# Kernel optimization log

Hardware: AMD Instinct MI355X
Metric: run time of the kernel (lower is better)

The kernel has to match this reference:

```python
import jax, jax.numpy as jnp
import numpy as np

IN_F = 2048
OUT_F = 2048
G = 5 + 3  # grid_size + spline_order
BATCH = 8192


def setup_inputs() -> dict:
    key = jax.random.key(0)
    k1, k2, k3 = jax.random.split(key, 3)
    x = jax.random.normal(k1, (BATCH, IN_F), dtype=jnp.float32)
    # kaiming_uniform(a=sqrt(5)) on (out,in): bound = 1/sqrt(in)
    bound = 1.0 / np.sqrt(IN_F)
    base_weight = jax.random.uniform(k2, (OUT_F, IN_F), dtype=jnp.float32,
                                     minval=-bound, maxval=bound)
    grid = 0.1 * jax.random.normal(k3, (IN_F, OUT_F, G), dtype=jnp.float32)
    return {"x": x, "base_weight": base_weight, "grid": grid}


def reference(x, base_weight, grid):
    # base branch: standard linear  (B, out)
    base_out = x @ base_weight.T
    # spline branch: Gaussian basis around the scalar grid mean  (B, in)
    basis = jnp.exp(-jnp.square(x - grid.mean()))
    # contract over in_features and the grid dim: sum_i sum_g basis[b,i]*grid[i,o,g]
    spline_out = basis @ grid.sum(axis=-1)  # (B, out)
    return base_out + spline_out
```

## Files before the change

kernel.cpp:

```cpp
#include <hip/hip_runtime.h>

#define IN_F   2048
#define OUT_F  2048
#define GDIM   8
#define BATCH  8192
#define KDIM   4096
#define GRID_TOTAL_INV (1.0f / 33554432.0f)

#define BK     32
#define NT     (KDIM / BK)
#define SLOT   32768
#define ATILE  16384

typedef __bf16 bf16x8 __attribute__((ext_vector_type(8)));
typedef float  f32x4  __attribute__((ext_vector_type(4)));
typedef unsigned short u16x8 __attribute__((ext_vector_type(8)));

__device__ __forceinline__ unsigned short f2bf(float f) {
  union { float f; unsigned int u; } v; v.f = f;
  unsigned int r = v.u + 0x7fffu + ((v.u >> 16) & 1u);
  return (unsigned short)(r >> 16);
}

__device__ __forceinline__ void gload_lds16(const void* g, void* l) {
  __builtin_amdgcn_global_load_lds(
      (const __attribute__((address_space(1))) void*)g,
      (__attribute__((address_space(3))) void*)l, 16, 0, 0);
}

template<int VM>
__device__ __forceinline__ void wait_vm() {
  if constexpr (VM == 12)     asm volatile("s_waitcnt vmcnt(12)" ::: "memory");
  else if constexpr (VM == 8) asm volatile("s_waitcnt vmcnt(8)"  ::: "memory");
  else if constexpr (VM == 4) asm volatile("s_waitcnt vmcnt(4)"  ::: "memory");
  else                        asm volatile("s_waitcnt vmcnt(0)"  ::: "memory");
}

__global__ __launch_bounds__(256) void prep_bw(const float* __restrict__ bw,
                                               unsigned short* __restrict__ Bt,
                                               float* __restrict__ sum_ptr) {
  if (blockIdx.x == 0 && threadIdx.x == 0) *sum_ptr = 0.0f;
  size_t i8 = ((size_t)blockIdx.x * 256 + threadIdx.x) * 8;
  const float4* p = reinterpret_cast<const float4*>(bw + i8);
  float4 a = p[0], b = p[1];
  u16x8 v;
  v[0] = f2bf(a.x); v[1] = f2bf(a.y); v[2] = f2bf(a.z); v[3] = f2bf(a.w);
  v[4] = f2bf(b.x); v[5] = f2bf(b.y); v[6] = f2bf(b.z); v[7] = f2bf(b.w);
  size_t o = i8 >> 11;
  size_t k = i8 & 2047;
  *reinterpret_cast<u16x8*>(Bt + o * KDIM + k) = v;
}

__global__ __launch_bounds__(256) void prep_grid(const float* __restrict__ grid,
                                                 unsigned short* __restrict__ Bt,
                                                 float* __restrict__ sum_ptr) {
  __shared__ float tile[32][33];
  __shared__ float wsum[4];
  int bi = blockIdx.x >> 6;
  int bo = blockIdx.x & 63;
  int i0 = bi << 5, o0 = bo << 5;
  int t = threadIdx.x;
  float local = 0.f;
#pragma unroll
  for (int p = 0; p < 4; ++p) {
    int li = t + 256 * p;
    int il = li >> 5, ol = li & 31;
    const float4* g4 = reinterpret_cast<const float4*>(
        grid + ((size_t)(i0 + il) * OUT_F + (size_t)(o0 + ol)) * GDIM);
    float4 a = g4[0], b = g4[1];
    float s = ((a.x + a.y) + (a.z + a.w)) + ((b.x + b.y) + (b.z + b.w));
    tile[il][ol] = s;
    local += s;
  }
#pragma unroll
  for (int off = 32; off >= 1; off >>= 1) local += __shfl_down(local, off, 64);
  int lane = t & 63, w = t >> 6;
  if (lane == 0) wsum[w] = local;
  __syncthreads();
#pragma unroll
  for (int p = 0; p < 4; ++p) {
    int li = t + 256 * p;
    int ol = li >> 5, il = li & 31;
    Bt[(size_t)(o0 + ol) * KDIM + IN_F + (i0 + il)] = f2bf(tile[il][ol]);
  }
  if (t == 0) atomicAdd(sum_ptr, (wsum[0] + wsum[1]) + (wsum[2] + wsum[3]));
}

__global__ __launch_bounds__(256) void prep_A(const float* __restrict__ x,
                                              const float* __restrict__ sum_ptr,
                                              unsigned short* __restrict__ Abuf) {
  float m = *sum_ptr * GRID_TOTAL_INV;
  size_t i8 = ((size_t)blockIdx.x * 256 + threadIdx.x) * 8;
  const float4* p = reinterpret_cast<const float4*>(x + i8);
  float4 a = p[0], b = p[1];
  float xs[8] = {a.x, a.y, a.z, a.w, b.x, b.y, b.z, b.w};
  u16x8 xv, bv;
#pragma unroll
  for (int j = 0; j < 8; ++j) {
    xv[j] = f2bf(xs[j]);
    float d = xs[j] - m;
    bv[j] = f2bf(__expf(-d * d));
  }
  size_t bi = i8 >> 11;
  size_t k  = i8 & 2047;
  *reinterpret_cast<u16x8*>(Abuf + bi * KDIM + k) = xv;
  *reinterpret_cast<u16x8*>(Abuf + bi * KDIM + IN_F + k) = bv;
}

__global__ __launch_bounds__(512, 2) void gemm_kernel(
    const unsigned short* __restrict__ A,
    const unsigned short* __restrict__ B,
    float* __restrict__ C) {
  __shared__ __align__(16) char lds[4 * SLOT];
  const int t    = threadIdx.x;
  const int lane = t & 63;
  const int wid  = t >> 6;
  const int wm   = wid >> 2;
  const int wn   = wid & 3;
  const int bx = blockIdx.x;
  const int bm = ((bx & 7) << 2) | ((bx >> 3) & 3);
  const int bn = bx >> 5;

  f32x4 acc[8][4] = {};

  const int cs = (t & 3) ^ ((t >> 4) & 3);
  const unsigned short* aSrc = A + ((size_t)(bm * 256 + (t >> 2)) * KDIM) + cs * 8;
  const unsigned short* bSrc = B + ((size_t)(bn * 256 + (t >> 2)) * KDIM) + cs * 8;
  const int dstOff = t * 16;

  const int swz = (lane >> 2) & 3;
  const int aRd = (wm * 128 + (lane & 15)) * 64 + (((lane >> 4) ^ swz) * 16);
  const int bRd = (wn * 64  + (lane & 15)) * 64 + (((lane >> 4) ^ swz) * 16);

  auto STAGE = [&](int tile) {
    const int slot = (tile & 3) * SLOT;
    const unsigned short* a = aSrc + tile * BK;
    const unsigned short* b = bSrc + tile * BK;
    gload_lds16(a,                        lds + slot + dstOff);
    gload_lds16(a + 128 * KDIM,           lds + slot + 8192 + dstOff);
    gload_lds16(b,                        lds + slot + ATILE + dstOff);
    gload_lds16(b + 128 * KDIM,           lds + slot + ATILE + 8192 + dstOff);
  };

  auto BODY = [&](int slotbase) {
    __builtin_amdgcn_sched_barrier(0);
    const char* sa = lds + slotbase + aRd;
    const char* sb = lds + slotbase + ATILE + bRd;
    bf16x8 af[8], bf[4];
#pragma unroll
    for (int m = 0; m < 8; ++m)
      af[m] = *reinterpret_cast<const bf16x8*>(sa + m * 1024);
#pragma unroll
    for (int n = 0; n < 4; ++n)
      bf[n] = *reinterpret_cast<const bf16x8*>(sb + n * 1024);
    asm volatile("s_waitcnt lgkmcnt(0)" ::: "memory");
    __builtin_amdgcn_sched_barrier(0);
    __builtin_amdgcn_s_barrier();
    __builtin_amdgcn_s_setprio(1);
#pragma unroll
    for (int m = 0; m < 8; ++m)
#pragma unroll
      for (int n = 0; n < 4; ++n)
        acc[m][n] = __builtin_amdgcn_mfma_f32_16x16x32_bf16(af[m], bf[n], acc[m][n], 0, 0, 0);
    __builtin_amdgcn_s_setprio(0);
  };

  STAGE(0); STAGE(1); STAGE(2);

  for (int kt = 0; kt < NT - 3; ++kt) {
    STAGE(kt + 3);
    wait_vm<12>();
    __builtin_amdgcn_s_barrier();
    BODY((kt & 3) * SLOT);
  }
  wait_vm<8>(); __builtin_amdgcn_s_barrier(); BODY(((NT - 3) & 3) * SLOT);
  wait_vm<4>(); __builtin_amdgcn_s_barrier(); BODY(((NT - 2) & 3) * SLOT);
  wait_vm<0>(); __builtin_amdgcn_s_barrier(); BODY(((NT - 1) & 3) * SLOT);

  const int rg = lane >> 4, cc = lane & 15;
  const size_t crow0 = (size_t)bm * 256 + wm * 128;
  const size_t ccol0 = (size_t)bn * 256 + wn * 64;
#pragma unroll
  for (int m = 0; m < 8; ++m)
#pragma unroll
    for (int n = 0; n < 4; ++n)
#pragma unroll
      for (int rr = 0; rr < 4; ++rr) {
        size_t row = crow0 + (size_t)m * 16 + rg * 4 + rr;
        size_t col = ccol0 + (size_t)n * 16 + cc;
        C[row * OUT_F + col] = acc[m][n][rr];
      }
}

extern "C" void kernel_launch(void* const* d_in, const int* in_sizes, int n_in,
                              void* d_out, int out_size, void* d_ws, size_t ws_size,
                              hipStream_t stream) {
  const float* x    = (const float*)d_in[0];
  const float* bw   = (const float*)d_in[1];
  const float* grid = (const float*)d_in[2];
  float* out = (float*)d_out;

  unsigned short* Abuf = (unsigned short*)d_ws;
  unsigned short* Bt   = Abuf + (size_t)BATCH * KDIM;
  float* sum_ptr = (float*)(Bt + (size_t)OUT_F * KDIM);

  prep_bw  <<<(OUT_F * IN_F / 8) / 256, 256, 0, stream>>>(bw, Bt, sum_ptr);
  prep_grid<<<64 * 64,                  256, 0, stream>>>(grid, Bt, sum_ptr);
  prep_A   <<<(BATCH * IN_F / 8) / 256, 256, 0, stream>>>(x, sum_ptr, Abuf);
  gemm_kernel<<<256, 512, 0, stream>>>(Abuf, Bt, out);
}
```

Measured before the change: 416.5 us.

## Restructure GEMM mainloop into double-buffered BK=64 pipeline with interleaved LDS reads

Replaces the 4-slot BK=32 ring buffer with two 64KB buffers holding BK=64 tiles, each split into two 32-wide subregions. Global-to-LDS loads for the next tile are interleaved with the ds_reads and MFMA quarters of the current tile, and A fragments are read in halves to cut register use. The intent is to halve the barriers per K element and overlap memory issue with compute more finely. The catch is a shallower prefetch depth (one tile ahead) and more complex vmcnt accounting, which could hurt correctness or latency hiding.

```diff
diff --git a/kernel.cpp b/kernel.cpp
--- a/kernel.cpp
+++ b/kernel.cpp
@@ -7,10 +7,11 @@
 #define KDIM   4096
 #define GRID_TOTAL_INV (1.0f / 33554432.0f)
 
-#define BK     32
-#define NT     (KDIM / BK)
-#define SLOT   32768
-#define ATILE  16384
+#define BK     64
+#define NKT    (KDIM / BK)
+#define BUFSZ  65536
+#define BOFF   32768
+#define REG    16384
 
 typedef __bf16 bf16x8 __attribute__((ext_vector_type(8)));
 typedef float  f32x4  __attribute__((ext_vector_type(4)));
@@ -26,14 +27,6 @@
   __builtin_amdgcn_global_load_lds(
       (const __attribute__((address_space(1))) void*)g,
       (__attribute__((address_space(3))) void*)l, 16, 0, 0);
-}
-
-template<int VM>
-__device__ __forceinline__ void wait_vm() {
-  if constexpr (VM == 12)     asm volatile("s_waitcnt vmcnt(12)" ::: "memory");
-  else if constexpr (VM == 8) asm volatile("s_waitcnt vmcnt(8)"  ::: "memory");
-  else if constexpr (VM == 4) asm volatile("s_waitcnt vmcnt(4)"  ::: "memory");
-  else                        asm volatile("s_waitcnt vmcnt(0)"  ::: "memory");
 }
 
 __global__ __launch_bounds__(256) void prep_bw(const float* __restrict__ bw,
@@ -111,7 +104,7 @@
     const unsigned short* __restrict__ A,
     const unsigned short* __restrict__ B,
     float* __restrict__ C) {
-  __shared__ __align__(16) char lds[4 * SLOT];
+  __shared__ __align__(16) char lds[2 * BUFSZ];
   const int t    = threadIdx.x;
   const int lane = t & 63;
   const int wid  = t >> 6;
@@ -122,60 +115,87 @@
   const int bn = bx >> 5;
 
   f32x4 acc[8][4] = {};
+  bf16x8 af[4], bf[4];
 
   const int cs = (t & 3) ^ ((t >> 4) & 3);
-  const unsigned short* aSrc = A + ((size_t)(bm * 256 + (t >> 2)) * KDIM) + cs * 8;
-  const unsigned short* bSrc = B + ((size_t)(bn * 256 + (t >> 2)) * KDIM) + cs * 8;
-  const int dstOff = t * 16;
-
-  const int swz = (lane >> 2) & 3;
-  const int aRd = (wm * 128 + (lane & 15)) * 64 + (((lane >> 4) ^ swz) * 16);
-  const int bRd = (wn * 64  + (lane & 15)) * 64 + (((lane >> 4) ^ swz) * 16);
-
-  auto STAGE = [&](int tile) {
-    const int slot = (tile & 3) * SLOT;
-    const unsigned short* a = aSrc + tile * BK;
-    const unsigned short* b = bSrc + tile * BK;
-    gload_lds16(a,                        lds + slot + dstOff);
-    gload_lds16(a + 128 * KDIM,           lds + slot + 8192 + dstOff);
-    gload_lds16(b,                        lds + slot + ATILE + dstOff);
-    gload_lds16(b + 128 * KDIM,           lds + slot + ATILE + 8192 + dstOff);
-  };
-
-  auto BODY = [&](int slotbase) {
-    __builtin_amdgcn_sched_barrier(0);
-    const char* sa = lds + slotbase + aRd;
-    const char* sb = lds + slotbase + ATILE + bRd;
-    bf16x8 af[8], bf[4];
-#pragma unroll
-    for (int m = 0; m < 8; ++m)
-      af[m] = *reinterpret_cast<const bf16x8*>(sa + m * 1024);
-#pragma unroll
-    for (int n = 0; n < 4; ++n)
-      bf[n] = *reinterpret_cast<const bf16x8*>(sb + n * 1024);
-    asm volatile("s_waitcnt lgkmcnt(0)" ::: "memory");
-    __builtin_amdgcn_sched_barrier(0);
-    __builtin_amdgcn_s_barrier();
-    __builtin_amdgcn_s_setprio(1);
-#pragma unroll
-    for (int m = 0; m < 8; ++m)
-#pragma unroll
-      for (int n = 0; n < 4; ++n)
-        acc[m][n] = __builtin_amdgcn_mfma_f32_16x16x32_bf16(af[m], bf[n], acc[m][n], 0, 0, 0);
-    __builtin_amdgcn_s_setprio(0);
-  };
-
-  STAGE(0); STAGE(1); STAGE(2);
-
-  for (int kt = 0; kt < NT - 3; ++kt) {
-    STAGE(kt + 3);
-    wait_vm<12>();
-    __builtin_amdgcn_s_barrier();
-    BODY((kt & 3) * SLOT);
-  }
-  wait_vm<8>(); __builtin_amdgcn_s_barrier(); BODY(((NT - 3) & 3) * SLOT);
-  wait_vm<4>(); __builtin_amdgcn_s_barrier(); BODY(((NT - 2) & 3) * SLOT);
-  wait_vm<0>(); __builtin_amdgcn_s_barrier(); BODY(((NT - 1) & 3) * SLOT);
+  const unsigned short* aStage = A + ((size_t)(bm * 256 + (t >> 2)) * KDIM) + cs * 8;
+  const unsigned short* bStage = B + ((size_t)(bn * 256 + (t >> 2)) * KDIM) + cs * 8;
+  const int dOff = t * 16;
+
+  const int sc  = (lane >> 4) ^ ((lane >> 2) & 3);
+  const int aRd = (wm * 128 + (lane & 15)) * 64 + sc * 16;
+  const int bRd = (wn * 64  + (lane & 15)) * 64 + sc * 16;
+
+#define STAGE_R(wb, kt, opOff, kk, src)                                        \
+  gload_lds16((src) + (size_t)(kt) * BK + (kk) * 32,                           \
+              (wb) + (opOff) + (kk) * REG + dOff);                             \
+  gload_lds16((src) + 128 * KDIM + (size_t)(kt) * BK + (kk) * 32,              \
+              (wb) + (opOff) + (kk) * REG + 8192 + dOff);
+
+#define DSREAD_A(rb, kk, mb)                                                   \
+  _Pragma("unroll")                                                            \
+  for (int i_ = 0; i_ < 4; ++i_)                                               \
+    af[i_] = *reinterpret_cast<const bf16x8*>(                                 \
+        (rb) + (kk) * REG + aRd + ((mb) + i_) * 1024);
+
+#define DSREAD_B(rb, kk)                                                       \
+  _Pragma("unroll")                                                            \
+  for (int n_ = 0; n_ < 4; ++n_)                                               \
+    bf[n_] = *reinterpret_cast<const bf16x8*>(                                 \
+        (rb) + BOFF + (kk) * REG + bRd + n_ * 1024);
+
+#define LGKM0                                                                  \
+  asm volatile("s_waitcnt lgkmcnt(0)" ::: "memory");                           \
+  __builtin_amdgcn_sched_barrier(0);
+
+#define MFMAQ(mb)                                                              \
+  __builtin_amdgcn_s_setprio(1);                                               \
+  _Pragma("unroll")                                                            \
+  for (int i_ = 0; i_ < 4; ++i_)                                               \
+    _Pragma("unroll")                                                          \
+    for (int n_ = 0; n_ < 4; ++n_)                                             \
+      acc[(mb) + i_][n_] = __builtin_amdgcn_mfma_f32_16x16x32_bf16(            \
+          af[i_], bf[n_], acc[(mb) + i_][n_], 0, 0, 0);                        \
+  __builtin_amdgcn_s_setprio(0);
+
+#define VMCNT(n) asm volatile("s_waitcnt vmcnt(" #n ")" ::: "memory");
+
+  STAGE_R(lds, 0, 0,    0, aStage);
+  STAGE_R(lds, 0, BOFF, 0, bStage);
+  STAGE_R(lds, 0, 0,    1, aStage);
+  STAGE_R(lds, 0, BOFF, 1, bStage);
+
+  for (int kt = 0; kt < NKT - 1; ++kt) {
+    const char* rb = lds + (kt & 1) * BUFSZ;
+    char* wb = lds + ((kt + 1) & 1) * BUFSZ;
+    STAGE_R(wb, kt + 1, 0, 0, aStage);
+    VMCNT(6);
+    __builtin_amdgcn_s_barrier();
+    DSREAD_A(rb, 0, 0); DSREAD_B(rb, 0);
+    LGKM0; MFMAQ(0);
+    DSREAD_A(rb, 0, 4);
+    STAGE_R(wb, kt + 1, BOFF, 0, bStage);
+    LGKM0; MFMAQ(4);
+    STAGE_R(wb, kt + 1, 0, 1, aStage);
+    VMCNT(6);
+    __builtin_amdgcn_s_barrier();
+    DSREAD_A(rb, 1, 0); DSREAD_B(rb, 1);
+    LGKM0; MFMAQ(0);
+    DSREAD_A(rb, 1, 4);
+    STAGE_R(wb, kt + 1, BOFF, 1, bStage);
+    LGKM0; MFMAQ(4);
+  }
+  {
+    const char* rb = lds + ((NKT - 1) & 1) * BUFSZ;
+    VMCNT(4);
+    __builtin_amdgcn_s_barrier();
+    DSREAD_A(rb, 0, 0); DSREAD_B(rb, 0); LGKM0; MFMAQ(0);
+    DSREAD_A(rb, 0, 4);                  LGKM0; MFMAQ(4);
+    VMCNT(0);
+    __builtin_amdgcn_s_barrier();
+    DSREAD_A(rb, 1, 0); DSREAD_B(rb, 1); LGKM0; MFMAQ(0);
+    DSREAD_A(rb, 1, 4);                  LGKM0; MFMAQ(4);
+  }
 
   const int rg = lane >> 4, cc = lane & 15;
   const size_t crow0 = (size_t)bm * 256 + wm * 128;
```

After: 398.2 us. -4.4%, faster.
